# Kernel optimization log

Hardware: AMD Instinct MI355X
Metric: run time of the kernel (lower is better)

Reference implementation:

```python
import jax, jax.numpy as jnp
import numpy as np

N_NODES = 50000
N_EDGES = 600000
IN_C = 128
HID = 128
OUT_C = 32
N_GRAPHS = 64


def setup_inputs() -> dict:
    key = jax.random.key(0)
    ks = jax.random.split(key, 12)
    x = jax.random.normal(ks[0], (N_NODES, IN_C), dtype=jnp.float32)
    edge_index = jax.random.randint(ks[1], (2, N_EDGES), 0, N_NODES, dtype=jnp.int64)
    batch = jnp.sort(jax.random.randint(ks[2], (N_NODES,), 0, N_GRAPHS, dtype=jnp.int64))
    s1 = 1.0 / np.sqrt(IN_C)
    s2 = 1.0 / np.sqrt(HID)
    # SAGEConv: out = lin_l(mean_neighbors) + lin_r(x); lin_l has bias, lin_r has none
    W1l = jax.random.uniform(ks[3], (HID, IN_C), minval=-s1, maxval=s1, dtype=jnp.float32)
    b1 = jax.random.uniform(ks[4], (HID,), minval=-s1, maxval=s1, dtype=jnp.float32)
    W1r = jax.random.uniform(ks[5], (HID, IN_C), minval=-s1, maxval=s1, dtype=jnp.float32)
    W2l = jax.random.uniform(ks[6], (HID, HID), minval=-s2, maxval=s2, dtype=jnp.float32)
    b2 = jax.random.uniform(ks[7], (HID,), minval=-s2, maxval=s2, dtype=jnp.float32)
    W2r = jax.random.uniform(ks[8], (HID, HID), minval=-s2, maxval=s2, dtype=jnp.float32)
    Wlin = jax.random.uniform(ks[9], (OUT_C, HID), minval=-s2, maxval=s2, dtype=jnp.float32)
    blin = jax.random.uniform(ks[10], (OUT_C,), minval=-s2, maxval=s2, dtype=jnp.float32)
    return {"x": x, "edge_index": edge_index, "batch": batch,
            "W1l": W1l, "b1": b1, "W1r": W1r,
            "W2l": W2l, "b2": b2, "W2r": W2r,
            "Wlin": Wlin, "blin": blin}


def _sage_conv(x, src, dst, Wl, bl, Wr):
    # mean aggregation of source-node features onto destination nodes
    msg_sum = jax.ops.segment_sum(x[src], dst, num_segments=N_NODES)  # [N, d]
    deg = jax.ops.segment_sum(jnp.ones((src.shape[0],), x.dtype), dst, num_segments=N_NODES)
    mean = msg_sum / jnp.maximum(deg, 1.0)[:, None]
    return mean @ Wl.T + bl + x @ Wr.T


def reference(x, edge_index, batch, W1l, b1, W1r, W2l, b2, W2r, Wlin, blin):
    src, dst = edge_index[0], edge_index[1]
    h = jax.nn.relu(_sage_conv(x, src, dst, W1l, b1, W1r))
    h = jax.nn.relu(_sage_conv(h, src, dst, W2l, b2, W2r))
    # global mean pool over graph ids
    gsum = jax.ops.segment_sum(h, batch, num_segments=N_GRAPHS)        # [G, HID]
    cnt = jax.ops.segment_sum(jnp.ones((h.shape[0],), h.dtype), batch, num_segments=N_GRAPHS)
    pooled = gsum / jnp.maximum(cnt, 1.0)[:, None]
    return pooled @ Wlin.T + blin
```

## Files before the change

kernel.cpp:

```cpp
#include <hip/hip_runtime.h>
#include <hip/hip_fp16.h>

#define N_NODES 50000
#define N_EDGES 600000
#define N_GRAPHS 64
#define HID 128
#define OUT_C 32

#define N_SCAN_BLOCKS ((N_NODES + 255) / 256)
#define SCAN_FLAG 0x40000000

typedef __attribute__((ext_vector_type(8))) _Float16 half8;
typedef __attribute__((ext_vector_type(4))) float f32x4;

#define ZERO_INTS (2 * N_NODES + N_SCAN_BLOCKS + N_GRAPHS * HID)

__global__ __launch_bounds__(256) void zero_kernel(int* __restrict__ zb) {
    int i = blockIdx.x * 256 + threadIdx.x;
    if (i < ZERO_INTS) zb[i] = 0;
}

#define DEG_BLOCKS ((N_EDGES + 255) / 256)
#define GST_BLOCKS ((N_NODES + 256) / 256)

__global__ __launch_bounds__(256) void deg_gst_w(
    const int* __restrict__ dst, int* __restrict__ degi,
    const int* __restrict__ batch, int* __restrict__ gstart,
    const float* __restrict__ W1l, const float* __restrict__ W1r,
    const float* __restrict__ W2l, const float* __restrict__ W2r,
    __half* __restrict__ Wt1, __half* __restrict__ Wt2) {
    const int b = blockIdx.x;
    const int t = threadIdx.x;
    if (b < DEG_BLOCKS) {
        int e = b * 256 + t;
        if (e < N_EDGES) atomicAdd(&degi[dst[e]], 1);
    } else if (b < DEG_BLOCKS + GST_BLOCKS) {
        int i = (b - DEG_BLOCKS) * 256 + t;
        if (i <= N_NODES) {
            if (i == 0) {
                int b1 = batch[0];
                for (int g = 0; g <= b1; ++g) gstart[g] = 0;
            } else if (i == N_NODES) {
                int b0 = batch[N_NODES - 1];
                for (int g = b0 + 1; g <= N_GRAPHS; ++g) gstart[g] = N_NODES;
            } else {
                int b0 = batch[i - 1], b1 = batch[i];
                for (int g = b0 + 1; g <= b1; ++g) gstart[g] = i;
            }
        }
    } else {
        int local = (b - DEG_BLOCKS - GST_BLOCKS) * 256 + t;
        for (int i = local; i < 65536; i += 4096) {
            int which = i >> 15;
            int j = i & 32767;
            int n = j >> 8, k = j & 255;
            const float* Wl = which ? W2l : W1l;
            const float* Wr = which ? W2r : W1r;
            float a = (k < 128) ? Wl[n * 128 + k] : Wr[n * 128 + (k - 128)];
            (which ? Wt2 : Wt1)[j] = __float2half(a);
        }
    }
}

__global__ __launch_bounds__(256) void scan_fused(
    const int* __restrict__ deg, int* __restrict__ bsum,
    int* __restrict__ rowptr, float* __restrict__ invdeg) {
    __shared__ int s[256];
    const int b = blockIdx.x;
    const int t = threadIdx.x;
    const int idx = b * 256 + t;
    const int v = (idx < N_NODES) ? deg[idx] : 0;
    s[t] = v;
    __syncthreads();
    for (int off = 1; off < 256; off <<= 1) {
        int u = (t >= off) ? s[t - off] : 0;
        __syncthreads();
        s[t] += u;
        __syncthreads();
    }
    const int incl = s[t];
    if (t == 255) atomicExch(&bsum[b], incl | SCAN_FLAG);

    int pv = 0;
    if (t < 64) {
        for (int f = t; f < b; f += 64) {
            int w;
            while (!((w = atomicAdd(&bsum[f], 0)) & SCAN_FLAG)) {
                __builtin_amdgcn_s_sleep(2);
            }
            pv += w & ~SCAN_FLAG;
        }
        for (int off = 32; off > 0; off >>= 1) pv += __shfl_down(pv, off);
        if (t == 0) s[0] = pv;
    }
    __syncthreads();
    const int boffs = s[0];

    if (idx < N_NODES) {
        rowptr[idx] = boffs + incl - v;
        invdeg[idx] = 1.0f / fmaxf((float)v, 1.0f);
    }
    if (b == N_SCAN_BLOCKS - 1 && t == 255) rowptr[N_NODES] = boffs + incl;
}

__global__ __launch_bounds__(256) void fill_cast(
    const int* __restrict__ src, const int* __restrict__ dst,
    const int* __restrict__ rowptr, int* __restrict__ cursor,
    int* __restrict__ eidx,
    const float* __restrict__ x, __half* __restrict__ xh) {
    const int b = blockIdx.x;
    const int t = threadIdx.x;
    if (b < DEG_BLOCKS) {
        int e = b * 256 + t;
        if (e < N_EDGES) {
            int d = dst[e];
            int pos = atomicAdd(&cursor[d], 1);
            eidx[rowptr[d] + pos] = src[e];
        }
    } else {
        int i = ((b - DEG_BLOCKS) * 256 + t) * 4;
        if (i < N_NODES * 128) {
            float4 v = *(const float4*)(x + i);
            __half2 a = __floats2half2_rn(v.x, v.y);
            __half2 c = __floats2half2_rn(v.z, v.w);
            uint2 st;
            st.x = *(const unsigned int*)&a;
            st.y = *(const unsigned int*)&c;
            *(uint2*)(xh + i) = st;
        }
    }
}

#define GBM 64

__global__ __launch_bounds__(256, 2) void sage_fused(
    const __half* __restrict__ feat16, const int* __restrict__ rowptr,
    const int* __restrict__ eidx, const float* __restrict__ invdeg,
    const __half* __restrict__ Wt, const float* __restrict__ bias,
    __half* __restrict__ out16,
    const int* __restrict__ batch, float* __restrict__ pooled,
    int M, int do_pool) {
    __shared__ __align__(16) __half Bs[128 * 256];
    __shared__ __align__(16) __half Ms[64 * 128];

    const int tid = threadIdx.x;
    const int wave = tid >> 6;
    const int lane = tid & 63;
    const int l15 = lane & 15;
    const int quad = lane >> 4;
    const int row0 = blockIdx.x * GBM;

    for (int id = tid; id < 128 * 32; id += 256) {
        int n = id >> 5;
        int kc16 = (id & 31) * 16;
        int off = (n * 512 + kc16) ^ ((n & 7) << 4);
        *(half8*)((char*)Bs + off) = *(const half8*)((const char*)Wt + n * 512 + kc16);
    }

    const int g16 = tid >> 4;
    const int sub = tid & 15;
    const int gbase = lane & 48;
    const size_t coff = (size_t)sub * 8;

    int begq[4], endq[4], pre0q[4], pre1q[4];
#pragma unroll
    for (int q = 0; q < 4; ++q) {
        int node = row0 + g16 + 16 * q;
        int bq = 0, eq = 0;
        if (node < M) { bq = rowptr[node]; eq = rowptr[node + 1]; }
        begq[q] = bq; endq[q] = eq;
    }
#pragma unroll
    for (int q = 0; q < 4; ++q) {
        int bq = begq[q], eq = endq[q];
        pre0q[q] = (eq > bq) ? eidx[min(bq + sub,      eq - 1)] : 0;
        pre1q[q] = (eq > bq) ? eidx[min(bq + 16 + sub, eq - 1)] : 0;
    }

    half8 vc[16];
#pragma unroll
    for (int k = 0; k < 16; ++k) {
        int id0 = __shfl(pre0q[0], gbase + k);
        vc[k] = *(const half8*)(feat16 + (size_t)id0 * 128 + coff);
    }

#pragma unroll
    for (int q = 0; q < 4; ++q) {
        const int nloc = g16 + 16 * q;
        const int node = row0 + nloc;
        const int beg = begq[q], end = endq[q];
        const int deg = end - beg;

        half8 vn[16];
        if (q < 3) {
#pragma unroll
            for (int k = 0; k < 16; ++k) {
                int idn = __shfl(pre0q[q + 1], gbase + k);
                vn[k] = *(const half8*)(feat16 + (size_t)idn * 128 + coff);
            }
        }

        float4 a[4], bb[4];
#pragma unroll
        for (int g = 0; g < 4; ++g) { a[g] = (float4){0.f,0.f,0.f,0.f}; bb[g] = (float4){0.f,0.f,0.f,0.f}; }

#pragma unroll
        for (int k = 0; k < 16; ++k) {
            const float w = (k < deg) ? 1.0f : 0.0f;
            const int g = k & 3;
            a[g].x  += w * (float)vc[k][0];
            a[g].y  += w * (float)vc[k][1];
            a[g].z  += w * (float)vc[k][2];
            a[g].w  += w * (float)vc[k][3];
            bb[g].x += w * (float)vc[k][4];
            bb[g].y += w * (float)vc[k][5];
            bb[g].z += w * (float)vc[k][6];
            bb[g].w += w * (float)vc[k][7];
        }

        for (int j0 = 16; j0 < deg; j0 += 16) {
            int idx[16];
            if (j0 == 16) {
#pragma unroll
                for (int k = 0; k < 16; ++k) idx[k] = __shfl(pre1q[q], gbase + k);
            } else {
#pragma unroll
                for (int k = 0; k < 16; ++k) idx[k] = eidx[min(beg + j0 + k, end - 1)];
            }
            half8 v[16];
#pragma unroll
            for (int k = 0; k < 16; ++k)
                v[k] = *(const half8*)(feat16 + (size_t)idx[k] * 128 + coff);
            const int rem = deg - j0;
#pragma unroll
            for (int k = 0; k < 16; ++k) {
                const float w = (k < rem) ? 1.0f : 0.0f;
                const int g = k & 3;
                a[g].x  += w * (float)v[k][0];
                a[g].y  += w * (float)v[k][1];
                a[g].z  += w * (float)v[k][2];
                a[g].w  += w * (float)v[k][3];
                bb[g].x += w * (float)v[k][4];
                bb[g].y += w * (float)v[k][5];
                bb[g].z += w * (float)v[k][6];
                bb[g].w += w * (float)v[k][7];
            }
        }

        const float sc = (node < M) ? invdeg[node] : 1.0f;
        half8 r;
        r[0] = (_Float16)(((a[0].x + a[1].x) + (a[2].x + a[3].x)) * sc);
        r[1] = (_Float16)(((a[0].y + a[1].y) + (a[2].y + a[3].y)) * sc);
        r[2] = (_Float16)(((a[0].z + a[1].z) + (a[2].z + a[3].z)) * sc);
        r[3] = (_Float16)(((a[0].w + a[1].w) + (a[2].w + a[3].w)) * sc);
        r[4] = (_Float16)(((bb[0].x + bb[1].x) + (bb[2].x + bb[3].x)) * sc);
        r[5] = (_Float16)(((bb[0].y + bb[1].y) + (bb[2].y + bb[3].y)) * sc);
        r[6] = (_Float16)(((bb[0].z + bb[1].z) + (bb[2].z + bb[3].z)) * sc);
        r[7] = (_Float16)(((bb[0].w + bb[1].w) + (bb[2].w + bb[3].w)) * sc);
        int moff = (nloc * 256 + (int)sub * 16) ^ ((nloc & 7) << 4);
        *(half8*)((char*)Ms + moff) = r;

        if (q < 3) {
#pragma unroll
            for (int k = 0; k < 16; ++k) vc[k] = vn[k];
        }
    }

    __syncthreads();

    const int arow = wave * 16 + l15;
    const int gi_a = min(row0 + arow, M - 1);
    half8 af[8];
#pragma unroll
    for (int kb = 0; kb < 4; ++kb) {
        int off = (arow * 256 + kb * 64 + quad * 16) ^ ((arow & 7) << 4);
        af[kb] = *(const half8*)((const char*)Ms + off);
    }
#pragma unroll
    for (int kb = 4; kb < 8; ++kb) {
        af[kb] = *(const half8*)(feat16 + (size_t)gi_a * 128 + (kb - 4) * 32 + quad * 8);
    }

    f32x4 acc[8];
#pragma unroll
    for (int t = 0; t < 8; ++t) acc[t] = (f32x4){0.f, 0.f, 0.f, 0.f};

#pragma unroll
    for (int kb = 0; kb < 8; ++kb) {
#pragma unroll
        for (int t = 0; t < 8; ++t) {
            const int n = t * 16 + l15;
            const int boff = (n * 512 + kb * 64 + quad * 16) ^ ((n & 7) << 4);
            const half8 b = *(const half8*)((const char*)Bs + boff);
            acc[t] = __builtin_amdgcn_mfma_f32_16x16x32_f16(af[kb], b, acc[t], 0, 0, 0);
        }
    }

    if (!do_pool) {
#pragma unroll
        for (int r = 0; r < 4; ++r) {
            int gi = row0 + wave * 16 + quad * 4 + r;
            if (gi < M) {
#pragma unroll
                for (int t = 0; t < 8; ++t) {
                    int col = t * 16 + l15;
                    float v = fmaxf(acc[t][r] + bias[col], 0.f);
                    out16[(size_t)gi * 128 + col] = __float2half(v);
                }
            }
        }
    } else {
        __syncthreads();
#pragma unroll
        for (int r = 0; r < 4; ++r) {
            int lrow = wave * 16 + quad * 4 + r;
            int gi = row0 + lrow;
#pragma unroll
            for (int t = 0; t < 8; ++t) {
                int col = t * 16 + l15;
                float v = fmaxf(acc[t][r] + bias[col], 0.f);
                if (gi >= M) v = 0.f;
                int off = (lrow * 256 + col * 2) ^ ((lrow & 7) << 4);
                *(__half*)((char*)Ms + off) = __float2half(v);
            }
        }
        __syncthreads();
        if (tid < 128) {
            const int col = tid;
            int cur = batch[min(row0, M - 1)];
            float s = 0.f;
            for (int r = 0; r < 64; ++r) {
                int gr = batch[min(row0 + r, M - 1)];
                if (gr != cur) {
                    atomicAdd(&pooled[cur * 128 + col], s);
                    s = 0.f; cur = gr;
                }
                int off = (r * 256 + col * 2) ^ ((r & 7) << 4);
                s += __half2float(*(const __half*)((const char*)Ms + off));
            }
            atomicAdd(&pooled[cur * 128 + col], s);
        }
    }
}

__global__ void final_kernel(const float* __restrict__ pooled,
                             const int* __restrict__ gstart,
                             const float* __restrict__ Wlin, const float* __restrict__ blin,
                             float* __restrict__ out) {
    int g = blockIdx.x;
    int j = threadIdx.x;
    float inv = 1.0f / fmaxf((float)(gstart[g + 1] - gstart[g]), 1.0f);
    float sum = blin[j];
    const float* w = Wlin + j * 128;
    const float* p = pooled + (size_t)g * 128;
    for (int c = 0; c < 128; ++c) {
        sum += p[c] * inv * w[c];
    }
    out[g * 32 + j] = sum;
}

extern "C" void kernel_launch(void* const* d_in, const int* in_sizes, int n_in,
                              void* d_out, int out_size, void* d_ws, size_t ws_size,
                              hipStream_t stream) {
    const float* x    = (const float*)d_in[0];
    const int*   src  = (const int*)d_in[1];
    const int*   dst  = ((const int*)d_in[1]) + N_EDGES;
    const int*   batch= (const int*)d_in[2];
    const float* W1l  = (const float*)d_in[3];
    const float* b1   = (const float*)d_in[4];
    const float* W1r  = (const float*)d_in[5];
    const float* W2l  = (const float*)d_in[6];
    const float* b2   = (const float*)d_in[7];
    const float* W2r  = (const float*)d_in[8];
    const float* Wlin = (const float*)d_in[9];
    const float* blin = (const float*)d_in[10];
    float* out = (float*)d_out;

    __half* xh     = (__half*)d_ws;
    __half* h1_16  = xh + 6400000;
    __half* Wt1    = h1_16 + 6400000;
    __half* Wt2    = Wt1 + 32768;
    float* invdeg  = (float*)(Wt2 + 32768);
    int*   gstart  = (int*)(invdeg + N_NODES);
    int*   degi    = gstart + 65;
    int*   cursor  = degi + N_NODES;
    int*   bsum    = cursor + N_NODES;
    float* pooled  = (float*)(bsum + N_SCAN_BLOCKS);
    int*   rowptr  = (int*)(pooled + N_GRAPHS*HID);
    int*   eidx    = rowptr + N_NODES + 1;

    zero_kernel<<<(ZERO_INTS + 255) / 256, 256, 0, stream>>>(degi);

    deg_gst_w<<<DEG_BLOCKS + GST_BLOCKS + 16, 256, 0, stream>>>(
        dst, degi, batch, gstart, W1l, W1r, W2l, W2r, Wt1, Wt2);

    scan_fused<<<N_SCAN_BLOCKS, 256, 0, stream>>>(degi, bsum, rowptr, invdeg);

    fill_cast<<<DEG_BLOCKS + (N_NODES * 128 / 4 + 255) / 256, 256, 0, stream>>>(
        src, dst, rowptr, cursor, eidx, x, xh);

    const int grid = (N_NODES + GBM - 1) / GBM;

    sage_fused<<<grid, 256, 0, stream>>>(
        xh, rowptr, eidx, invdeg, Wt1, b1, h1_16, batch, pooled, N_NODES, 0);

    sage_fused<<<grid, 256, 0, stream>>>(
        h1_16, rowptr, eidx, invdeg, Wt2, b2, (__half*)0, batch, pooled, N_NODES, 1);

    final_kernel<<<N_GRAPHS, 32, 0, stream>>>(pooled, gstart, Wlin, blin, out);
}
```

Measured before the change: 253.0 us.

## Merge preprocessing kernels into one persistent kernel with software grid barriers

Replaces the separate degree/gstart/weight-cast, scan, and fill/cast kernels with a single persistent kernel of 512 blocks that uses atomic-counter grid barriers between phases. The scan becomes a three-phase block-scan, block-prefix, fixup instead of decoupled lookback. The goal is to remove kernel launch gaps and the spin-waiting in the scan. The cost is grid-stride loops with fewer threads, and the barriers rely on all 512 blocks being co-resident or the kernel deadlocks.

```diff
diff --git a/kernel.cpp b/kernel.cpp
--- a/kernel.cpp
+++ b/kernel.cpp
@@ -8,126 +8,121 @@
 #define OUT_C 32
 
 #define N_SCAN_BLOCKS ((N_NODES + 255) / 256)
-#define SCAN_FLAG 0x40000000
+#define PREP_BLOCKS 512
 
 typedef __attribute__((ext_vector_type(8))) _Float16 half8;
 typedef __attribute__((ext_vector_type(4))) float f32x4;
 
-#define ZERO_INTS (2 * N_NODES + N_SCAN_BLOCKS + N_GRAPHS * HID)
+#define ZERO_INTS (2 * N_NODES + 2 * N_SCAN_BLOCKS + 4 + N_GRAPHS * HID)
 
 __global__ __launch_bounds__(256) void zero_kernel(int* __restrict__ zb) {
     int i = blockIdx.x * 256 + threadIdx.x;
     if (i < ZERO_INTS) zb[i] = 0;
 }
 
-#define DEG_BLOCKS ((N_EDGES + 255) / 256)
-#define GST_BLOCKS ((N_NODES + 256) / 256)
-
-__global__ __launch_bounds__(256) void deg_gst_w(
-    const int* __restrict__ dst, int* __restrict__ degi,
-    const int* __restrict__ batch, int* __restrict__ gstart,
+__device__ __forceinline__ void grid_barrier(int* cnt) {
+    __syncthreads();
+    if (threadIdx.x == 0) {
+        __threadfence();
+        atomicAdd(cnt, 1);
+        while (atomicAdd(cnt, 0) < PREP_BLOCKS) __builtin_amdgcn_s_sleep(2);
+        __threadfence();
+    }
+    __syncthreads();
+}
+
+__global__ __launch_bounds__(256, 2) void prep_mega(
+    const int* __restrict__ src, const int* __restrict__ dst, const int* __restrict__ batch,
     const float* __restrict__ W1l, const float* __restrict__ W1r,
     const float* __restrict__ W2l, const float* __restrict__ W2r,
-    __half* __restrict__ Wt1, __half* __restrict__ Wt2) {
-    const int b = blockIdx.x;
+    __half* __restrict__ Wt1, __half* __restrict__ Wt2,
+    const float* __restrict__ x, __half* __restrict__ xh,
+    int* __restrict__ degi, int* __restrict__ cursor,
+    int* __restrict__ bsum, int* __restrict__ bpre, int* __restrict__ ctrB,
+    int* __restrict__ gstart, int* __restrict__ rowptr, float* __restrict__ invdeg,
+    int* __restrict__ eidx) {
+    const int bid = blockIdx.x;
     const int t = threadIdx.x;
-    if (b < DEG_BLOCKS) {
-        int e = b * 256 + t;
-        if (e < N_EDGES) atomicAdd(&degi[dst[e]], 1);
-    } else if (b < DEG_BLOCKS + GST_BLOCKS) {
-        int i = (b - DEG_BLOCKS) * 256 + t;
-        if (i <= N_NODES) {
-            if (i == 0) {
-                int b1 = batch[0];
-                for (int g = 0; g <= b1; ++g) gstart[g] = 0;
-            } else if (i == N_NODES) {
-                int b0 = batch[N_NODES - 1];
-                for (int g = b0 + 1; g <= N_GRAPHS; ++g) gstart[g] = N_NODES;
-            } else {
-                int b0 = batch[i - 1], b1 = batch[i];
-                for (int g = b0 + 1; g <= b1; ++g) gstart[g] = i;
-            }
-        }
-    } else {
-        int local = (b - DEG_BLOCKS - GST_BLOCKS) * 256 + t;
-        for (int i = local; i < 65536; i += 4096) {
-            int which = i >> 15;
-            int j = i & 32767;
-            int n = j >> 8, k = j & 255;
-            const float* Wl = which ? W2l : W1l;
-            const float* Wr = which ? W2r : W1r;
-            float a = (k < 128) ? Wl[n * 128 + k] : Wr[n * 128 + (k - 128)];
-            (which ? Wt2 : Wt1)[j] = __float2half(a);
-        }
-    }
-}
-
-__global__ __launch_bounds__(256) void scan_fused(
-    const int* __restrict__ deg, int* __restrict__ bsum,
-    int* __restrict__ rowptr, float* __restrict__ invdeg) {
+    const int gtid = bid * 256 + t;
+    const int gsz = PREP_BLOCKS * 256;
     __shared__ int s[256];
-    const int b = blockIdx.x;
-    const int t = threadIdx.x;
-    const int idx = b * 256 + t;
-    const int v = (idx < N_NODES) ? deg[idx] : 0;
-    s[t] = v;
-    __syncthreads();
-    for (int off = 1; off < 256; off <<= 1) {
-        int u = (t >= off) ? s[t - off] : 0;
+
+    for (int e = gtid; e < N_EDGES; e += gsz) atomicAdd(&degi[dst[e]], 1);
+    for (int i = gtid; i <= N_NODES; i += gsz) {
+        if (i == 0) {
+            int b1 = batch[0];
+            for (int g = 0; g <= b1; ++g) gstart[g] = 0;
+        } else if (i == N_NODES) {
+            int b0 = batch[N_NODES - 1];
+            for (int g = b0 + 1; g <= N_GRAPHS; ++g) gstart[g] = N_NODES;
+        } else {
+            int b0 = batch[i - 1], b1 = batch[i];
+            for (int g = b0 + 1; g <= b1; ++g) gstart[g] = i;
+        }
+    }
+    for (int i = gtid; i < 65536; i += gsz) {
+        int which = i >> 15;
+        int j = i & 32767;
+        int n = j >> 8, k = j & 255;
+        const float* Wl = which ? W2l : W1l;
+        const float* Wr = which ? W2r : W1r;
+        float a = (k < 128) ? Wl[n * 128 + k] : Wr[n * 128 + (k - 128)];
+        (which ? Wt2 : Wt1)[j] = __float2half(a);
+    }
+    grid_barrier(&ctrB[0]);
+
+    if (bid < N_SCAN_BLOCKS) {
+        const int c = bid;
+        const int idx = c * 256 + t;
+        const int v = (idx < N_NODES) ? degi[idx] : 0;
+        s[t] = v;
         __syncthreads();
-        s[t] += u;
+        for (int off = 1; off < 256; off <<= 1) {
+            int u = (t >= off) ? s[t - off] : 0;
+            __syncthreads();
+            s[t] += u;
+            __syncthreads();
+        }
+        if (idx < N_NODES) rowptr[idx] = s[t];
+        if (t == 255) bsum[c] = s[255];
+    }
+    grid_barrier(&ctrB[1]);
+
+    if (bid == 0) {
+        const int v = (t < N_SCAN_BLOCKS) ? bsum[t] : 0;
+        s[t] = v;
         __syncthreads();
-    }
-    const int incl = s[t];
-    if (t == 255) atomicExch(&bsum[b], incl | SCAN_FLAG);
-
-    int pv = 0;
-    if (t < 64) {
-        for (int f = t; f < b; f += 64) {
-            int w;
-            while (!((w = atomicAdd(&bsum[f], 0)) & SCAN_FLAG)) {
-                __builtin_amdgcn_s_sleep(2);
-            }
-            pv += w & ~SCAN_FLAG;
-        }
-        for (int off = 32; off > 0; off >>= 1) pv += __shfl_down(pv, off);
-        if (t == 0) s[0] = pv;
-    }
-    __syncthreads();
-    const int boffs = s[0];
-
-    if (idx < N_NODES) {
-        rowptr[idx] = boffs + incl - v;
-        invdeg[idx] = 1.0f / fmaxf((float)v, 1.0f);
-    }
-    if (b == N_SCAN_BLOCKS - 1 && t == 255) rowptr[N_NODES] = boffs + incl;
-}
-
-__global__ __launch_bounds__(256) void fill_cast(
-    const int* __restrict__ src, const int* __restrict__ dst,
-    const int* __restrict__ rowptr, int* __restrict__ cursor,
-    int* __restrict__ eidx,
-    const float* __restrict__ x, __half* __restrict__ xh) {
-    const int b = blockIdx.x;
-    const int t = threadIdx.x;
-    if (b < DEG_BLOCKS) {
-        int e = b * 256 + t;
-        if (e < N_EDGES) {
-            int d = dst[e];
-            int pos = atomicAdd(&cursor[d], 1);
-            eidx[rowptr[d] + pos] = src[e];
-        }
-    } else {
-        int i = ((b - DEG_BLOCKS) * 256 + t) * 4;
-        if (i < N_NODES * 128) {
-            float4 v = *(const float4*)(x + i);
-            __half2 a = __floats2half2_rn(v.x, v.y);
-            __half2 c = __floats2half2_rn(v.z, v.w);
-            uint2 st;
-            st.x = *(const unsigned int*)&a;
-            st.y = *(const unsigned int*)&c;
-            *(uint2*)(xh + i) = st;
-        }
+        for (int off = 1; off < 256; off <<= 1) {
+            int u = (t >= off) ? s[t - off] : 0;
+            __syncthreads();
+            s[t] += u;
+            __syncthreads();
+        }
+        if (t < N_SCAN_BLOCKS) bpre[t] = s[t] - v;
+    }
+    grid_barrier(&ctrB[2]);
+
+    for (int i = gtid; i < N_NODES; i += gsz) {
+        int d = degi[i];
+        rowptr[i] = rowptr[i] + bpre[i >> 8] - d;
+        invdeg[i] = 1.0f / fmaxf((float)d, 1.0f);
+    }
+    if (gtid == 0) rowptr[N_NODES] = N_EDGES;
+    grid_barrier(&ctrB[3]);
+
+    for (int e = gtid; e < N_EDGES; e += gsz) {
+        int d = dst[e];
+        int pos = atomicAdd(&cursor[d], 1);
+        eidx[rowptr[d] + pos] = src[e];
+    }
+    for (int i = gtid; i < N_NODES * 128 / 4; i += gsz) {
+        float4 v = *(const float4*)(x + (size_t)i * 4);
+        __half2 a = __floats2half2_rn(v.x, v.y);
+        __half2 c = __floats2half2_rn(v.z, v.w);
+        uint2 st;
+        st.x = *(const unsigned int*)&a;
+        st.y = *(const unsigned int*)&c;
+        *(uint2*)(xh + (size_t)i * 4) = st;
     }
 }
 
@@ -385,19 +380,17 @@
     int*   degi    = gstart + 65;
     int*   cursor  = degi + N_NODES;
     int*   bsum    = cursor + N_NODES;
-    float* pooled  = (float*)(bsum + N_SCAN_BLOCKS);
+    int*   bpre    = bsum + N_SCAN_BLOCKS;
+    int*   ctrB    = bpre + N_SCAN_BLOCKS;
+    float* pooled  = (float*)(ctrB + 4);
     int*   rowptr  = (int*)(pooled + N_GRAPHS*HID);
     int*   eidx    = rowptr + N_NODES + 1;
 
     zero_kernel<<<(ZERO_INTS + 255) / 256, 256, 0, stream>>>(degi);
 
-    deg_gst_w<<<DEG_BLOCKS + GST_BLOCKS + 16, 256, 0, stream>>>(
-        dst, degi, batch, gstart, W1l, W1r, W2l, W2r, Wt1, Wt2);
-
-    scan_fused<<<N_SCAN_BLOCKS, 256, 0, stream>>>(degi, bsum, rowptr, invdeg);
-
-    fill_cast<<<DEG_BLOCKS + (N_NODES * 128 / 4 + 255) / 256, 256, 0, stream>>>(
-        src, dst, rowptr, cursor, eidx, x, xh);
+    prep_mega<<<PREP_BLOCKS, 256, 0, stream>>>(
+        src, dst, batch, W1l, W1r, W2l, W2r, Wt1, Wt2, x, xh,
+        degi, cursor, bsum, bpre, ctrB, gstart, rowptr, invdeg, eidx);
 
     const int grid = (N_NODES + GBM - 1) / GBM;
 
```

New measurement: 405.6 us. 60.3% more time.
